# Optimization experiments

Hardware: AMD Instinct MI355X
Metric: run time of the kernel (lower is better)

## Reference

```python
import jax, jax.numpy as jnp
import numpy as np
import math

BS, S, DIM, H = 2, 2048, 1024, 16
DH = DIM // H


def setup_inputs() -> dict:
    key = jax.random.key(0)
    ks = jax.random.split(key, 11)
    std = 1.0 / math.sqrt(DIM)
    inp = {
        "query": jax.random.normal(ks[0], (BS, S, DIM), jnp.float32),
        "key_": jax.random.normal(ks[1], (BS, S, DIM), jnp.float32),
        "value": jax.random.normal(ks[2], (BS, S, DIM), jnp.float32),
        "mask": jnp.ones((BS, S), jnp.int32),
        "q_w": jax.random.normal(ks[3], (DIM, DIM), jnp.float32) * std,
        "q_b": jnp.zeros((DIM,), jnp.float32),
        "k_w": jax.random.normal(ks[4], (DIM, DIM), jnp.float32) * std,
        "k_b": jnp.zeros((DIM,), jnp.float32),
        "v_w": jax.random.normal(ks[5], (DIM, DIM), jnp.float32) * std,
        "v_b": jnp.zeros((DIM,), jnp.float32),
        "o_w": jax.random.normal(ks[6], (DIM, DIM), jnp.float32) * std,
        "o_b": jnp.zeros((DIM,), jnp.float32),
    }
    return inp


def _shape(x):
    # (bs, s, dim) -> (bs, h, s, dh)
    return x.reshape(BS, -1, H, DH).transpose(0, 2, 1, 3)


def reference(query, key_, value, mask, q_w, q_b, k_w, k_b, v_w, v_b, o_w, o_b):
    # linear projections (torch Linear: x @ W.T + b)
    q = _shape(query @ q_w.T + q_b) / math.sqrt(DH)
    k = _shape(key_ @ k_w.T + k_b)
    v = _shape(value @ v_w.T + v_b)
    # scores: (bs, h, s, s)
    scores = jnp.einsum("bhqd,bhkd->bhqk", q, k)
    pad = (mask == 0)[:, None, None, :]  # (bs,1,1,k_len)
    scores = jnp.where(pad, -jnp.inf, scores)
    weights = jax.nn.softmax(scores, axis=-1)
    context = jnp.einsum("bhqk,bhkd->bhqd", weights, v)
    context = context.transpose(0, 2, 1, 3).reshape(BS, -1, DIM)
    return context @ o_w.T + o_b
```

## Files before the change

kernel.cpp:

```cpp
#include <hip/hip_runtime.h>
#include <hip/hip_bf16.h>

#define BSZ 2
#define SEQ 2048
#define DIMN 1024
#define NH 16
#define DH 64
#define LOG2E 1.4426950408889634f

typedef unsigned short ushort_t;
typedef __attribute__((ext_vector_type(8))) short short8;
typedef __attribute__((ext_vector_type(4))) float float4v;

__device__ __forceinline__ ushort_t f2bf(float f) {
    union { float f; unsigned int u; } c; c.f = f;
    return (ushort_t)((c.u + 0x8000u) >> 16);
}
__device__ __forceinline__ unsigned int pkbf(float a, float b) {
    __hip_bfloat162 h = __float22bfloat162_rn(make_float2(a, b));
    unsigned int u; __builtin_memcpy(&u, &h, 4); return u;
}
__device__ __forceinline__ void gld16(const ushort_t* g, ushort_t* l) {
    __builtin_amdgcn_global_load_lds(
        (const __attribute__((address_space(1))) unsigned int*)g,
        (__attribute__((address_space(3))) unsigned int*)l, 16, 0, 0);
}

__global__ __launch_bounds__(256) void cvt_w(
    const float* __restrict__ w0, const float* __restrict__ w1,
    const float* __restrict__ w2, const float* __restrict__ w3,
    ushort_t* __restrict__ o0, ushort_t* __restrict__ o1,
    ushort_t* __restrict__ o2, ushort_t* __restrict__ o3)
{
    const float* s; ushort_t* d;
    switch (blockIdx.y) {
        case 0: s = w0; d = o0; break;
        case 1: s = w1; d = o1; break;
        case 2: s = w2; d = o2; break;
        default: s = w3; d = o3; break;
    }
    int i = (blockIdx.x * 256 + threadIdx.x) * 4;
    float4v v = *(const float4v*)(s + i);
    uint2 o; o.x = pkbf(v[0], v[1]); o.y = pkbf(v[2], v[3]);
    *(uint2*)(d + i) = o;
}

__global__ __launch_bounds__(256) void gemm_qkv(
    const float* __restrict__ xq, const float* __restrict__ xk, const float* __restrict__ xv,
    const ushort_t* __restrict__ Wq, const ushort_t* __restrict__ Wk, const ushort_t* __restrict__ Wv,
    const float* __restrict__ qb, const float* __restrict__ kb, const float* __restrict__ vb,
    ushort_t* __restrict__ Qp, ushort_t* __restrict__ Kp, ushort_t* __restrict__ VpT)
{
    __shared__ ushort_t As[128 * 72];
    __shared__ ushort_t Bs[128 * 72];
    const int tid  = threadIdx.x;
    const int lane = tid & 63;
    const int w    = tid >> 6;
    const int wm   = w >> 1, wn = w & 1;
    const int quad = lane >> 4;
    const int l16  = lane & 15;
    const int mBase = blockIdx.y * 128;
    const int nGlob = blockIdx.x * 128;
    const int z     = nGlob >> 10;
    const int nBase = nGlob & 1023;
    const float*    A    = (z == 0) ? xq : (z == 1) ? xk : xv;
    const ushort_t* W    = (z == 0) ? Wq : (z == 1) ? Wk : Wv;
    const float*    bias = (z == 0) ? qb : (z == 1) ? kb : vb;

    float4v acc[4][4];
    const float4v z4 = {0.f, 0.f, 0.f, 0.f};
#pragma unroll
    for (int i = 0; i < 4; ++i)
#pragma unroll
        for (int j = 0; j < 4; ++j) acc[i][j] = z4;

    for (int k0 = 0; k0 < 1024; k0 += 64) {
        float4v a[4][2];
        short8  wb[4];
#pragma unroll
        for (int it = 0; it < 4; ++it) {
            int c = it * 256 + tid, row = c >> 3, col = (c & 7) * 8;
            const float* g = A + (size_t)(mBase + row) * 1024 + k0 + col;
            a[it][0] = *(const float4v*)g;
            a[it][1] = *(const float4v*)(g + 4);
            wb[it] = *(const short8*)(W + (size_t)(nBase + row) * 1024 + k0 + col);
        }
        __syncthreads();
#pragma unroll
        for (int it = 0; it < 4; ++it) {
            int c = it * 256 + tid, row = c >> 3, col = (c & 7) * 8;
            uint4 ua;
            ua.x = pkbf(a[it][0][0], a[it][0][1]); ua.y = pkbf(a[it][0][2], a[it][0][3]);
            ua.z = pkbf(a[it][1][0], a[it][1][1]); ua.w = pkbf(a[it][1][2], a[it][1][3]);
            *(uint4*)&As[row * 72 + col] = ua;
            *(short8*)&Bs[row * 72 + col] = wb[it];
        }
        __syncthreads();

#pragma unroll
        for (int ksub = 0; ksub < 2; ++ksub) {
            short8 af[4], bf[4];
#pragma unroll
            for (int mt = 0; mt < 4; ++mt)
                af[mt] = *(const short8*)&As[(wm * 64 + mt * 16 + l16) * 72 + ksub * 32 + quad * 8];
#pragma unroll
            for (int nt = 0; nt < 4; ++nt)
                bf[nt] = *(const short8*)&Bs[(wn * 64 + nt * 16 + l16) * 72 + ksub * 32 + quad * 8];
#pragma unroll
            for (int mt = 0; mt < 4; ++mt)
#pragma unroll
                for (int nt = 0; nt < 4; ++nt)
                    acc[mt][nt] = __builtin_amdgcn_mfma_f32_16x16x32_bf16(af[mt], bf[nt], acc[mt][nt], 0, 0, 0);
        }
    }

    const float scale = (z == 0) ? 0.125f * LOG2E : 1.0f;
    if (z < 2) {
        ushort_t* C = (z == 0) ? Qp : Kp;
#pragma unroll
        for (int mt = 0; mt < 4; ++mt)
#pragma unroll
            for (int nt = 0; nt < 4; ++nt) {
                int colg = nBase + wn * 64 + nt * 16 + l16;
                float bv = bias[colg];
#pragma unroll
                for (int r = 0; r < 4; ++r) {
                    int rowg = mBase + wm * 64 + mt * 16 + quad * 4 + r;
                    C[(size_t)rowg * 1024 + colg] = f2bf((acc[mt][nt][r] + bv) * scale);
                }
            }
    } else {
#pragma unroll
        for (int mt = 0; mt < 4; ++mt)
#pragma unroll
            for (int nt = 0; nt < 4; ++nt) {
                int n = nBase + wn * 64 + nt * 16 + l16;
                int hh = n >> 6, d = n & 63;
                float bv = bias[n];
                int rowg = mBase + wm * 64 + mt * 16 + quad * 4;
                int b = rowg >> 11, s = rowg & 2047;
                uint2 pk;
                pk.x = pkbf(acc[mt][nt][0] + bv, acc[mt][nt][1] + bv);
                pk.y = pkbf(acc[mt][nt][2] + bv, acc[mt][nt][3] + bv);
                *(uint2*)&VpT[(((size_t)(b * 16 + hh) * 64 + d) << 11) + s] = pk;
            }
    }
}

__global__ __launch_bounds__(256) void gemm_o(
    const ushort_t* __restrict__ A, const ushort_t* __restrict__ W,
    const float* __restrict__ bias, float* __restrict__ C)
{
    __shared__ ushort_t As[128 * 72];
    __shared__ ushort_t Bs[64 * 72];
    const int tid  = threadIdx.x;
    const int lane = tid & 63;
    const int w    = tid >> 6;
    const int wm   = w & 1, wn = w >> 1;
    const int quad = lane >> 4;
    const int l16  = lane & 15;
    const int mBase = blockIdx.y * 128;
    const int nBase = blockIdx.x * 64;

    float4v acc[4][2];
    const float4v z4 = {0.f, 0.f, 0.f, 0.f};
#pragma unroll
    for (int mt = 0; mt < 4; ++mt)
#pragma unroll
        for (int nt = 0; nt < 2; ++nt) acc[mt][nt] = z4;

    for (int k0 = 0; k0 < 1024; k0 += 64) {
        short8 ab[4], wb[2];
#pragma unroll
        for (int it = 0; it < 4; ++it) {
            int c = it * 256 + tid, row = c >> 3, col = (c & 7) * 8;
            ab[it] = *(const short8*)(A + (size_t)(mBase + row) * 1024 + k0 + col);
        }
#pragma unroll
        for (int it = 0; it < 2; ++it) {
            int c = it * 256 + tid, row = c >> 3, col = (c & 7) * 8;
            wb[it] = *(const short8*)(W + (size_t)(nBase + row) * 1024 + k0 + col);
        }
        __syncthreads();
#pragma unroll
        for (int it = 0; it < 4; ++it) {
            int c = it * 256 + tid, row = c >> 3, col = (c & 7) * 8;
            *(short8*)&As[row * 72 + col] = ab[it];
        }
#pragma unroll
        for (int it = 0; it < 2; ++it) {
            int c = it * 256 + tid, row = c >> 3, col = (c & 7) * 8;
            *(short8*)&Bs[row * 72 + col] = wb[it];
        }
        __syncthreads();

#pragma unroll
        for (int ksub = 0; ksub < 2; ++ksub) {
            short8 af[4], bf[2];
#pragma unroll
            for (int mt = 0; mt < 4; ++mt)
                af[mt] = *(const short8*)&As[(wm * 64 + mt * 16 + l16) * 72 + ksub * 32 + quad * 8];
#pragma unroll
            for (int nt = 0; nt < 2; ++nt)
                bf[nt] = *(const short8*)&Bs[(wn * 32 + nt * 16 + l16) * 72 + ksub * 32 + quad * 8];
#pragma unroll
            for (int mt = 0; mt < 4; ++mt)
#pragma unroll
                for (int nt = 0; nt < 2; ++nt)
                    acc[mt][nt] = __builtin_amdgcn_mfma_f32_16x16x32_bf16(af[mt], bf[nt], acc[mt][nt], 0, 0, 0);
        }
    }

#pragma unroll
    for (int mt = 0; mt < 4; ++mt)
#pragma unroll
        for (int nt = 0; nt < 2; ++nt) {
            int colg = nBase + wn * 32 + nt * 16 + l16;
            float bv = bias[colg];
#pragma unroll
            for (int r = 0; r < 4; ++r) {
                int rowg = mBase + wm * 64 + mt * 16 + quad * 4 + r;
                C[(size_t)rowg * 1024 + colg] = acc[mt][nt][r] + bv;
            }
        }
}

__global__ __launch_bounds__(512) void attn_kernel(
    const ushort_t* __restrict__ Qp, const ushort_t* __restrict__ Kp,
    const ushort_t* __restrict__ VpT, const int* __restrict__ mask,
    ushort_t* __restrict__ Cp)
{
    __shared__ __align__(16) ushort_t Qs[128 * 64];
    __shared__ __align__(16) ushort_t Ks[2][64 * 64];
    __shared__ __align__(16) ushort_t Vt[2][64 * 64];
    __shared__ int s_mok[8];

    const int tid  = threadIdx.x;
    const int lane = tid & 63;
    const int w    = tid >> 6;
    const int quad = lane >> 4;
    const int l16  = lane & 15;
    const int sw   = l16 & 7;
    const int b    = blockIdx.x >> 4;
    const int h    = blockIdx.x & 15;
    const int q0   = blockIdx.y * 128;

    const int srow = tid >> 3;
    const int sc   = tid & 7;
    const int gsc  = (sc ^ (srow & 7)) * 8;
    const ushort_t* Vbase = VpT + ((size_t)(b * 16 + h) * 64) * 2048;
    const ushort_t* Kbase = Kp + (size_t)b * SEQ * DIMN + h * DH;
    const ushort_t* Qbase = Qp + (size_t)(b * SEQ + q0) * DIMN + h * DH;

    {
        int m0 = mask[b * SEQ + tid];
        int m1 = mask[b * SEQ + 512 + tid];
        int m2 = mask[b * SEQ + 1024 + tid];
        int m3 = mask[b * SEQ + 1536 + tid];
        int ok = __all((m0 != 0) & (m1 != 0) & (m2 != 0) & (m3 != 0));
        if (lane == 0) s_mok[w] = ok;
    }

#pragma unroll
    for (int it2 = 0; it2 < 2; ++it2) {
        int row = it2 * 64 + srow;
        gld16(Qbase + (size_t)row * DIMN + ((sc ^ (row & 7)) * 8),
              &Qs[(it2 * 64 + w * 8) * 64]);
    }
    gld16(Kbase + (size_t)srow * DIMN + gsc, &Ks[0][w * 512]);
    gld16(Vbase + (size_t)srow * 2048 + gsc, &Vt[0][w * 512]);
    __syncthreads();

    const int mall = s_mok[0] & s_mok[1] & s_mok[2] & s_mok[3]
                   & s_mok[4] & s_mok[5] & s_mok[6] & s_mok[7];

    short8 bq[2];
#pragma unroll
    for (int ks = 0; ks < 2; ++ks)
        bq[ks] = *(const short8*)&Qs[(w * 16 + l16) * 64 + ((4 * ks + quad) ^ sw) * 8];

    const float4v z4 = {0.f, 0.f, 0.f, 0.f};
    float4v Oacc[4];
#pragma unroll
    for (int vt = 0; vt < 4; ++vt) Oacc[vt] = z4;
    float4v Lacc = z4;
    float mrow = 0.0f;
    float4v mneg4 = z4;

    short8 ones;
#pragma unroll
    for (int j = 0; j < 8; ++j) ones[j] = (short)0x3F80;

    const int NT = SEQ / 64;
    for (int it = 0; it < NT; ++it) {
        const int bsel = it & 1;
        const int kt0  = it * 64;

        if (it + 1 < NT) {
            int kn = kt0 + 64;
            gld16(Kbase + (size_t)(kn + srow) * DIMN + gsc, &Ks[bsel ^ 1][w * 512]);
            gld16(Vbase + (size_t)srow * 2048 + kn + gsc, &Vt[bsel ^ 1][w * 512]);
        }

        float4v Sv[4];
        __builtin_amdgcn_s_setprio(1);
#pragma unroll
        for (int kt = 0; kt < 4; ++kt) {
            short8 ak = *(const short8*)&Ks[bsel][(kt * 16 + l16) * 64 + (quad ^ sw) * 8];
            Sv[kt] = __builtin_amdgcn_mfma_f32_16x16x32_bf16(ak, bq[0], mneg4, 0, 0, 0);
        }
#pragma unroll
        for (int kt = 0; kt < 4; ++kt) {
            short8 ak = *(const short8*)&Ks[bsel][(kt * 16 + l16) * 64 + ((4 + quad) ^ sw) * 8];
            Sv[kt] = __builtin_amdgcn_mfma_f32_16x16x32_bf16(ak, bq[1], Sv[kt], 0, 0, 0);
        }
        __builtin_amdgcn_s_setprio(0);

        if (!mall) {
            int4 mv4[4];
#pragma unroll
            for (int kt = 0; kt < 4; ++kt)
                mv4[kt] = *(const int4*)(mask + b * SEQ + kt0 + kt * 16 + quad * 4);
#pragma unroll
            for (int kt = 0; kt < 4; ++kt) {
                int4 mv = mv4[kt];
#pragma unroll
                for (int r = 0; r < 4; ++r) {
                    int m = (r == 0) ? mv.x : (r == 1) ? mv.y : (r == 2) ? mv.z : mv.w;
                    Sv[kt][r] += (m == 0) ? -1e30f : 0.0f;
                }
            }
        }

        float t0 = fmaxf(fmaxf(Sv[0][0], Sv[0][1]), fmaxf(Sv[0][2], Sv[0][3]));
        float t1 = fmaxf(fmaxf(Sv[1][0], Sv[1][1]), fmaxf(Sv[1][2], Sv[1][3]));
        float t2 = fmaxf(fmaxf(Sv[2][0], Sv[2][1]), fmaxf(Sv[2][2], Sv[2][3]));
        float t3 = fmaxf(fmaxf(Sv[3][0], Sv[3][1]), fmaxf(Sv[3][2], Sv[3][3]));
        float mx = fmaxf(fmaxf(t0, t1), fmaxf(t2, t3));
        mx = fmaxf(mx, __shfl_xor(mx, 16));
        mx = fmaxf(mx, __shfl_xor(mx, 32));
        if (!__all(mx <= 8.0f)) {
            float d = fmaxf(mx, 0.0f);
            float alpha = exp2f(-d);
            mrow += d;
#pragma unroll
            for (int vt = 0; vt < 4; ++vt) Oacc[vt] *= alpha;
            Lacc *= alpha;
#pragma unroll
            for (int kt = 0; kt < 4; ++kt)
#pragma unroll
                for (int r = 0; r < 4; ++r) Sv[kt][r] -= d;
            mneg4[0] = -mrow; mneg4[1] = -mrow; mneg4[2] = -mrow; mneg4[3] = -mrow;
        }
#pragma unroll
        for (int kt = 0; kt < 4; ++kt)
#pragma unroll
            for (int r = 0; r < 4; ++r) Sv[kt][r] = exp2f(Sv[kt][r]);

#pragma unroll
        for (int kt = 0; kt < 4; ++kt) {
            uint2 pk;
            pk.x = pkbf(Sv[kt][0], Sv[kt][1]);
            pk.y = pkbf(Sv[kt][2], Sv[kt][3]);
            int chunk = (2 * kt + (quad >> 1)) ^ sw;
            *(uint2*)&Qs[(w * 16 + l16) * 64 + chunk * 8 + (quad & 1) * 4] = pk;
        }

        __builtin_amdgcn_s_setprio(1);
#pragma unroll
        for (int ks = 0; ks < 2; ++ks) {
            short8 bp = *(const short8*)&Qs[(w * 16 + l16) * 64 + ((4 * ks + quad) ^ sw) * 8];
            Lacc = __builtin_amdgcn_mfma_f32_16x16x32_bf16(ones, bp, Lacc, 0, 0, 0);
#pragma unroll
            for (int vt = 0; vt < 4; ++vt) {
                short8 av = *(const short8*)&Vt[bsel][(vt * 16 + l16) * 64 + ((4 * ks + quad) ^ sw) * 8];
                Oacc[vt] = __builtin_amdgcn_mfma_f32_16x16x32_bf16(av, bp, Oacc[vt], 0, 0, 0);
            }
        }
        __builtin_amdgcn_s_setprio(0);

        __syncthreads();
    }

    float inv = 1.0f / Lacc[0];
    int row = q0 + w * 16 + l16;
#pragma unroll
    for (int vt = 0; vt < 4; ++vt) {
        uint2 pk;
        pk.x = pkbf(Oacc[vt][0] * inv, Oacc[vt][1] * inv);
        pk.y = pkbf(Oacc[vt][2] * inv, Oacc[vt][3] * inv);
        *(uint2*)&Cp[(size_t)(b * SEQ + row) * DIMN + h * DH + vt * 16 + quad * 4] = pk;
    }
}

extern "C" void kernel_launch(void* const* d_in, const int* in_sizes, int n_in,
                              void* d_out, int out_size, void* d_ws, size_t ws_size,
                              hipStream_t stream) {
    const float* x_q = (const float*)d_in[0];
    const float* x_k = (const float*)d_in[1];
    const float* x_v = (const float*)d_in[2];
    const int*   msk = (const int*)d_in[3];
    const float* q_w = (const float*)d_in[4];
    const float* q_b = (const float*)d_in[5];
    const float* k_w = (const float*)d_in[6];
    const float* k_b = (const float*)d_in[7];
    const float* v_w = (const float*)d_in[8];
    const float* v_b = (const float*)d_in[9];
    const float* o_w = (const float*)d_in[10];
    const float* o_b = (const float*)d_in[11];
    float* out = (float*)d_out;

    const size_t NEL = (size_t)BSZ * SEQ * DIMN;
    const size_t WEL = (size_t)DIMN * DIMN;
    ushort_t* Qp  = (ushort_t*)d_ws;
    ushort_t* Kp  = Qp + NEL;
    ushort_t* VpT = Kp + NEL;
    ushort_t* Wq  = VpT + NEL;
    ushort_t* Wk  = Wq + WEL;
    ushort_t* Wv  = Wk + WEL;
    ushort_t* Wo  = Wv + WEL;
    ushort_t* Cp  = Qp;

    cvt_w<<<dim3(WEL / 1024, 4), 256, 0, stream>>>(q_w, k_w, v_w, o_w, Wq, Wk, Wv, Wo);
    gemm_qkv<<<dim3(24, 32), 256, 0, stream>>>(x_q, x_k, x_v, Wq, Wk, Wv,
                                               q_b, k_b, v_b, Qp, Kp, VpT);
    attn_kernel<<<dim3(BSZ * NH, SEQ / 128), 512, 0, stream>>>(Qp, Kp, VpT, msk, Cp);
    gemm_o<<<dim3(16, 32), 256, 0, stream>>>(Cp, Wo, o_b, out);
}
```

Before: 261.1 us.

## Pre-convert activations to bf16 and use direct-to-LDS QKV GEMM with inline asm softmax

Adds a conversion pass that casts the fp32 query/key/value inputs to bf16 in workspace. A new QKV GEMM then streams both operands with global_load_lds into XOR-swizzled shared memory, replacing fp32 register loads and in-kernel conversion. The attention kernel switches to raw v_exp_f32, v_max3_f32 and v_cvt_pk_bf16_f32 inline asm and unrolls its main loop by two. The fast path is taken only when the workspace is at least 56 MB, and it costs an extra full pass over the activations plus larger workspace traffic.

```diff
diff --git a/kernel.cpp b/kernel.cpp
--- a/kernel.cpp
+++ b/kernel.cpp
@@ -20,29 +20,58 @@
     __hip_bfloat162 h = __float22bfloat162_rn(make_float2(a, b));
     unsigned int u; __builtin_memcpy(&u, &h, 4); return u;
 }
+__device__ __forceinline__ unsigned int pkbf_asm(float a, float b) {
+    unsigned int d;
+    asm("v_cvt_pk_bf16_f32 %0, %1, %2" : "=v"(d) : "v"(a), "v"(b));
+    return d;
+}
+__device__ __forceinline__ float exp2_raw(float x) {
+    float d; asm("v_exp_f32 %0, %1" : "=v"(d) : "v"(x)); return d;
+}
+__device__ __forceinline__ float max3f(float a, float b, float c) {
+    float d; asm("v_max3_f32 %0, %1, %2, %3" : "=v"(d) : "v"(a), "v"(b), "v"(c)); return d;
+}
 __device__ __forceinline__ void gld16(const ushort_t* g, ushort_t* l) {
     __builtin_amdgcn_global_load_lds(
         (const __attribute__((address_space(1))) unsigned int*)g,
         (__attribute__((address_space(3))) unsigned int*)l, 16, 0, 0);
 }
 
-__global__ __launch_bounds__(256) void cvt_w(
+__global__ __launch_bounds__(256) void cvt_all(
     const float* __restrict__ w0, const float* __restrict__ w1,
     const float* __restrict__ w2, const float* __restrict__ w3,
+    const float* __restrict__ x0, const float* __restrict__ x1,
+    const float* __restrict__ x2,
     ushort_t* __restrict__ o0, ushort_t* __restrict__ o1,
-    ushort_t* __restrict__ o2, ushort_t* __restrict__ o3)
+    ushort_t* __restrict__ o2, ushort_t* __restrict__ o3,
+    ushort_t* __restrict__ xb)
 {
-    const float* s; ushort_t* d;
-    switch (blockIdx.y) {
-        case 0: s = w0; d = o0; break;
-        case 1: s = w1; d = o1; break;
-        case 2: s = w2; d = o2; break;
-        default: s = w3; d = o3; break;
-    }
-    int i = (blockIdx.x * 256 + threadIdx.x) * 4;
-    float4v v = *(const float4v*)(s + i);
-    uint2 o; o.x = pkbf(v[0], v[1]); o.y = pkbf(v[2], v[3]);
-    *(uint2*)(d + i) = o;
+    const int y = blockIdx.y;
+    if (y < 4) {
+        const float* s; ushort_t* d;
+        switch (y) {
+            case 0: s = w0; d = o0; break;
+            case 1: s = w1; d = o1; break;
+            case 2: s = w2; d = o2; break;
+            default: s = w3; d = o3; break;
+        }
+        int i = (blockIdx.x * 256 + threadIdx.x) * 4;
+        float4v v = *(const float4v*)(s + i);
+        uint2 o; o.x = pkbf(v[0], v[1]); o.y = pkbf(v[2], v[3]);
+        *(uint2*)(d + i) = o;
+    } else {
+        const int m = y - 4;
+        const float* s = (m == 0) ? x0 : (m == 1) ? x1 : x2;
+        ushort_t* d = xb + (size_t)m * (BSZ * SEQ * DIMN);
+        size_t base = (size_t)blockIdx.x * 4096;
+#pragma unroll
+        for (int j = 0; j < 4; ++j) {
+            size_t i = base + j * 1024 + threadIdx.x * 4;
+            float4v v = *(const float4v*)(s + i);
+            uint2 o; o.x = pkbf(v[0], v[1]); o.y = pkbf(v[2], v[3]);
+            *(uint2*)(d + i) = o;
+        }
+    }
 }
 
 __global__ __launch_bounds__(256) void gemm_qkv(
@@ -147,6 +176,100 @@
     }
 }
 
+__global__ __launch_bounds__(256) void gemm_qkv_fast(
+    const ushort_t* __restrict__ Xb,
+    const ushort_t* __restrict__ Wq, const ushort_t* __restrict__ Wk, const ushort_t* __restrict__ Wv,
+    const float* __restrict__ qb, const float* __restrict__ kb, const float* __restrict__ vb,
+    ushort_t* __restrict__ Qp, ushort_t* __restrict__ Kp, ushort_t* __restrict__ VpT)
+{
+    __shared__ __align__(16) ushort_t As[128 * 64];
+    __shared__ __align__(16) ushort_t Bs[128 * 64];
+    const int tid  = threadIdx.x;
+    const int lane = tid & 63;
+    const int w    = tid >> 6;
+    const int wm   = w >> 1, wn = w & 1;
+    const int quad = lane >> 4;
+    const int l16  = lane & 15;
+    const int sw   = l16 & 7;
+    const int mBase = blockIdx.y * 128;
+    const int nGlob = blockIdx.x * 128;
+    const int z     = nGlob >> 10;
+    const int nBase = nGlob & 1023;
+    const ushort_t* A    = Xb + (size_t)z * (BSZ * SEQ * DIMN);
+    const ushort_t* W    = (z == 0) ? Wq : (z == 1) ? Wk : Wv;
+    const float*    bias = (z == 0) ? qb : (z == 1) ? kb : vb;
+
+    const int srow = tid >> 3;
+    const int sc   = tid & 7;
+
+    float4v acc[4][4];
+    const float4v z4 = {0.f, 0.f, 0.f, 0.f};
+#pragma unroll
+    for (int i = 0; i < 4; ++i)
+#pragma unroll
+        for (int j = 0; j < 4; ++j) acc[i][j] = z4;
+
+    for (int k0 = 0; k0 < 1024; k0 += 64) {
+#pragma unroll
+        for (int itq = 0; itq < 4; ++itq) {
+            int row = itq * 32 + srow;
+            int colsw = (sc ^ (row & 7)) * 8;
+            gld16(A + (size_t)(mBase + row) * 1024 + k0 + colsw, &As[(itq * 32 + w * 8) * 64]);
+            gld16(W + (size_t)(nBase + row) * 1024 + k0 + colsw, &Bs[(itq * 32 + w * 8) * 64]);
+        }
+        __syncthreads();
+
+#pragma unroll
+        for (int ksub = 0; ksub < 2; ++ksub) {
+            short8 af[4], bf[4];
+#pragma unroll
+            for (int mt = 0; mt < 4; ++mt)
+                af[mt] = *(const short8*)&As[(wm * 64 + mt * 16 + l16) * 64 + ((ksub * 4 + quad) ^ sw) * 8];
+#pragma unroll
+            for (int nt = 0; nt < 4; ++nt)
+                bf[nt] = *(const short8*)&Bs[(wn * 64 + nt * 16 + l16) * 64 + ((ksub * 4 + quad) ^ sw) * 8];
+#pragma unroll
+            for (int mt = 0; mt < 4; ++mt)
+#pragma unroll
+                for (int nt = 0; nt < 4; ++nt)
+                    acc[mt][nt] = __builtin_amdgcn_mfma_f32_16x16x32_bf16(af[mt], bf[nt], acc[mt][nt], 0, 0, 0);
+        }
+        __syncthreads();
+    }
+
+    const float scale = (z == 0) ? 0.125f * LOG2E : 1.0f;
+    if (z < 2) {
+        ushort_t* C = (z == 0) ? Qp : Kp;
+#pragma unroll
+        for (int mt = 0; mt < 4; ++mt)
+#pragma unroll
+            for (int nt = 0; nt < 4; ++nt) {
+                int colg = nBase + wn * 64 + nt * 16 + l16;
+                float bv = bias[colg];
+#pragma unroll
+                for (int r = 0; r < 4; ++r) {
+                    int rowg = mBase + wm * 64 + mt * 16 + quad * 4 + r;
+                    C[(size_t)rowg * 1024 + colg] = f2bf((acc[mt][nt][r] + bv) * scale);
+                }
+            }
+    } else {
+#pragma unroll
+        for (int mt = 0; mt < 4; ++mt)
+#pragma unroll
+            for (int nt = 0; nt < 4; ++nt) {
+                int n = nBase + wn * 64 + nt * 16 + l16;
+                int hh = n >> 6, d = n & 63;
+                float bv = bias[n];
+                int rowg = mBase + wm * 64 + mt * 16 + quad * 4;
+                int b = rowg >> 11, s = rowg & 2047;
+                uint2 pk;
+                pk.x = pkbf(acc[mt][nt][0] + bv, acc[mt][nt][1] + bv);
+                pk.y = pkbf(acc[mt][nt][2] + bv, acc[mt][nt][3] + bv);
+                *(uint2*)&VpT[(((size_t)(b * 16 + hh) * 64 + d) << 11) + s] = pk;
+            }
+    }
+}
+
 __global__ __launch_bounds__(256) void gemm_o(
     const ushort_t* __restrict__ A, const ushort_t* __restrict__ W,
     const float* __restrict__ bias, float* __restrict__ C)
@@ -292,6 +415,7 @@
     for (int j = 0; j < 8; ++j) ones[j] = (short)0x3F80;
 
     const int NT = SEQ / 64;
+#pragma unroll 2
     for (int it = 0; it < NT; ++it) {
         const int bsel = it & 1;
         const int kt0  = it * 64;
@@ -332,16 +456,19 @@
             }
         }
 
-        float t0 = fmaxf(fmaxf(Sv[0][0], Sv[0][1]), fmaxf(Sv[0][2], Sv[0][3]));
-        float t1 = fmaxf(fmaxf(Sv[1][0], Sv[1][1]), fmaxf(Sv[1][2], Sv[1][3]));
-        float t2 = fmaxf(fmaxf(Sv[2][0], Sv[2][1]), fmaxf(Sv[2][2], Sv[2][3]));
-        float t3 = fmaxf(fmaxf(Sv[3][0], Sv[3][1]), fmaxf(Sv[3][2], Sv[3][3]));
-        float mx = fmaxf(fmaxf(t0, t1), fmaxf(t2, t3));
+        float a0 = max3f(Sv[0][0], Sv[0][1], Sv[0][2]);
+        float a1 = max3f(Sv[0][3], Sv[1][0], Sv[1][1]);
+        float a2 = max3f(Sv[1][2], Sv[1][3], Sv[2][0]);
+        float a3 = max3f(Sv[2][1], Sv[2][2], Sv[2][3]);
+        float a4 = max3f(Sv[3][0], Sv[3][1], Sv[3][2]);
+        float b0 = max3f(a0, a1, Sv[3][3]);
+        float b1 = max3f(a2, a3, a4);
+        float mx = fmaxf(b0, b1);
         mx = fmaxf(mx, __shfl_xor(mx, 16));
         mx = fmaxf(mx, __shfl_xor(mx, 32));
         if (!__all(mx <= 8.0f)) {
             float d = fmaxf(mx, 0.0f);
-            float alpha = exp2f(-d);
+            float alpha = exp2_raw(-d);
             mrow += d;
 #pragma unroll
             for (int vt = 0; vt < 4; ++vt) Oacc[vt] *= alpha;
@@ -355,13 +482,13 @@
 #pragma unroll
         for (int kt = 0; kt < 4; ++kt)
 #pragma unroll
-            for (int r = 0; r < 4; ++r) Sv[kt][r] = exp2f(Sv[kt][r]);
+            for (int r = 0; r < 4; ++r) Sv[kt][r] = exp2_raw(Sv[kt][r]);
 
 #pragma unroll
         for (int kt = 0; kt < 4; ++kt) {
             uint2 pk;
-            pk.x = pkbf(Sv[kt][0], Sv[kt][1]);
-            pk.y = pkbf(Sv[kt][2], Sv[kt][3]);
+            pk.x = pkbf_asm(Sv[kt][0], Sv[kt][1]);
+            pk.y = pkbf_asm(Sv[kt][2], Sv[kt][3]);
             int chunk = (2 * kt + (quad >> 1)) ^ sw;
             *(uint2*)&Qs[(w * 16 + l16) * 64 + chunk * 8 + (quad & 1) * 4] = pk;
         }
@@ -387,8 +514,8 @@
 #pragma unroll
     for (int vt = 0; vt < 4; ++vt) {
         uint2 pk;
-        pk.x = pkbf(Oacc[vt][0] * inv, Oacc[vt][1] * inv);
-        pk.y = pkbf(Oacc[vt][2] * inv, Oacc[vt][3] * inv);
+        pk.x = pkbf_asm(Oacc[vt][0] * inv, Oacc[vt][1] * inv);
+        pk.y = pkbf_asm(Oacc[vt][2] * inv, Oacc[vt][3] * inv);
         *(uint2*)&Cp[(size_t)(b * SEQ + row) * DIMN + h * DH + vt * 16 + quad * 4] = pk;
     }
 }
@@ -419,11 +546,21 @@
     ushort_t* Wk  = Wq + WEL;
     ushort_t* Wv  = Wk + WEL;
     ushort_t* Wo  = Wv + WEL;
+    ushort_t* Xb  = Wo + WEL;
     ushort_t* Cp  = Qp;
 
-    cvt_w<<<dim3(WEL / 1024, 4), 256, 0, stream>>>(q_w, k_w, v_w, o_w, Wq, Wk, Wv, Wo);
-    gemm_qkv<<<dim3(24, 32), 256, 0, stream>>>(x_q, x_k, x_v, Wq, Wk, Wv,
-                                               q_b, k_b, v_b, Qp, Kp, VpT);
+    const bool fast = ws_size >= ((size_t)56 << 20);
+    if (fast) {
+        cvt_all<<<dim3(1024, 7), 256, 0, stream>>>(q_w, k_w, v_w, o_w, x_q, x_k, x_v,
+                                                   Wq, Wk, Wv, Wo, Xb);
+        gemm_qkv_fast<<<dim3(24, 32), 256, 0, stream>>>(Xb, Wq, Wk, Wv,
+                                                        q_b, k_b, v_b, Qp, Kp, VpT);
+    } else {
+        cvt_all<<<dim3(1024, 4), 256, 0, stream>>>(q_w, k_w, v_w, o_w, x_q, x_k, x_v,
+                                                   Wq, Wk, Wv, Wo, Xb);
+        gemm_qkv<<<dim3(24, 32), 256, 0, stream>>>(x_q, x_k, x_v, Wq, Wk, Wv,
+                                                   q_b, k_b, v_b, Qp, Kp, VpT);
+    }
     attn_kernel<<<dim3(BSZ * NH, SEQ / 128), 512, 0, stream>>>(Qp, Kp, VpT, msk, Cp);
     gemm_o<<<dim3(16, 32), 256, 0, stream>>>(Cp, Wo, o_b, out);
 }
```

After: 227.4 us. -12.9%, faster.
